# Kernel optimization log

Hardware: AMD Instinct MI355X
Metric: run time of the kernel (lower is better)

## Reference

```python
import jax, jax.numpy as jnp
import numpy as np

N = 50000          # num nodes
E = 800000         # num edges
IN_C = 256
HID = 128
OUT_C = 2
R = 8              # num_relations
B = 4              # num_bases
L = 3              # n_layers
ALPHA = 0.1


def setup_inputs() -> dict:
    key = jax.random.key(0)
    ks = jax.random.split(key, 12)
    x = jax.random.normal(ks[0], (N, IN_C), dtype=jnp.float32)
    edge_index = jax.random.randint(ks[1], (2, E), 0, N, dtype=jnp.int64)
    edge_type = jax.random.randint(ks[2], (E,), 0, R, dtype=jnp.int64)
    # parameters
    lin1_w = jax.random.normal(ks[3], (IN_C, HID), dtype=jnp.float32) * (1.0 / np.sqrt(IN_C))
    lin1_b = jnp.zeros((HID,), dtype=jnp.float32)
    bases = jax.random.normal(ks[4], (L, B, HID, HID), dtype=jnp.float32) * (1.0 / np.sqrt(HID))
    comp = jax.random.normal(ks[5], (L, R, B), dtype=jnp.float32) * (1.0 / np.sqrt(B))
    root = jax.random.normal(ks[6], (L, HID, HID), dtype=jnp.float32) * (1.0 / np.sqrt(HID))
    bias_conv = jnp.zeros((L, HID), dtype=jnp.float32)
    lin2_w = jax.random.normal(ks[7], (HID, OUT_C), dtype=jnp.float32) * (1.0 / np.sqrt(HID))
    lin2_b = jnp.zeros((OUT_C,), dtype=jnp.float32)
    # GPR-style temp init: temp[k] = alpha*(1-alpha)^k, temp[K] = (1-alpha)^K
    temp = ALPHA * (1.0 - ALPHA) ** np.arange(L + 1)
    temp[-1] = (1.0 - ALPHA) ** L
    temp = jnp.asarray(temp, dtype=jnp.float32)
    return {"x": x, "edge_index": edge_index, "edge_type": edge_type,
            "lin1_w": lin1_w, "lin1_b": lin1_b, "bases": bases, "comp": comp,
            "root": root, "bias_conv": bias_conv, "lin2_w": lin2_w,
            "lin2_b": lin2_b, "temp": temp}


def rgcn_conv(x, bases_l, comp_l, root_l, bias_l, src, dst, edge_type):
    # basis decomposition: W_r = sum_b comp[r,b] * bases[b]   -> [R, HID, HID]
    W = jnp.einsum('rb,bio->rio', comp_l, bases_l)
    out = x @ root_l + bias_l                      # root/self transform + bias
    for r in range(R):                             # fixed small relation set
        mask = (edge_type == r)
        h = x @ W[r]                               # [N, HID] relation transform
        msg = jnp.where(mask[:, None], h[src], 0.0)  # [E, HID] gathered messages
        agg = jax.ops.segment_sum(msg, dst, num_segments=N)
        cnt = jax.ops.segment_sum(mask.astype(x.dtype), dst, num_segments=N)
        out = out + agg / jnp.maximum(cnt, 1.0)[:, None]   # mean aggregation
    return out


def reference(x, edge_index, edge_type, lin1_w, lin1_b, bases, comp, root,
              bias_conv, lin2_w, lin2_b, temp):
    src, dst = edge_index[0], edge_index[1]
    h = jax.nn.relu(x @ lin1_w + lin1_b)           # pre_transform=False path; dropout=identity (eval)
    hidden = h * temp[0]
    cur = hidden
    for i in range(L):
        cur = rgcn_conv(cur, bases[i], comp[i], root[i], bias_conv[i], src, dst, edge_type)
        if i < L - 1:
            cur = jax.nn.relu(cur)
        hidden = hidden + temp[i + 1] * cur
    return hidden @ lin2_w + lin2_b                # [N, OUT_C]
```

## Files before the change

### kernel.cpp

```cpp
#include <hip/hip_runtime.h>

#define Nn   50000
#define Ee   800000
#define INC  256
#define HIDd 128
#define RR   8
#define BB   4
#define LL   3
#define RN   (RR * Nn)
#define NCH  391

typedef _Float16 f16;
typedef _Float16 f16x2 __attribute__((ext_vector_type(2)));
typedef _Float16 f16x4 __attribute__((ext_vector_type(4)));
typedef _Float16 f16x8 __attribute__((ext_vector_type(8)));
typedef float    f32x4 __attribute__((ext_vector_type(4)));

static inline size_t align256(size_t x) { return (x + 255) & ~(size_t)255; }


__global__ void count_k(const int* __restrict__ ei, const int* __restrict__ et,
                        int* __restrict__ cnt) {
    int e = blockIdx.x * 256 + threadIdx.x;
    if (e < Ee) {
        int d = ei[Ee + e];
        int r = et[e];
        atomicAdd(&cnt[r * Nn + d], 1);
    }
}

__global__ __launch_bounds__(256) void chunksum_k(const int* __restrict__ cnt,
                                                  int* __restrict__ csum) {
    int c = blockIdx.x;
    int t = threadIdx.x;
    int idx4 = c * 256 + t;
    int s = 0;
    if (idx4 < RN / 4) {
        int4 v = ((const int4*)cnt)[idx4];
        s = v.x + v.y + v.z + v.w;
    }
#pragma unroll
    for (int o = 1; o < 64; o <<= 1) s += __shfl_xor(s, o);
    __shared__ int ws[4];
    if ((t & 63) == 0) ws[t >> 6] = s;
    __syncthreads();
    if (t == 0) csum[c] = ws[0] + ws[1] + ws[2] + ws[3];
}

__global__ __launch_bounds__(512) void chunkscan_k(const int* __restrict__ csum,
                                                   int* __restrict__ cbase,
                                                   int* __restrict__ off) {
    __shared__ int lds[NCH];
    int t = threadIdx.x;
    if (t < NCH) lds[t] = csum[t];
    __syncthreads();
    if (t == 0) {
        int run = 0;
        for (int i = 0; i < NCH; ++i) { int v = lds[i]; lds[i] = run; run += v; }
        off[RN] = run;
    }
    __syncthreads();
    if (t < NCH) cbase[t] = lds[t];
}

__global__ __launch_bounds__(256) void writeoff_k(const int* __restrict__ cnt,
                                                  const int* __restrict__ cbase,
                                                  int* __restrict__ off,
                                                  int* __restrict__ cursor,
                                                  float* __restrict__ invc) {
    int c = blockIdx.x;
    int t = threadIdx.x;
    int idx4 = c * 256 + t;
    bool ok = idx4 < RN / 4;
    int4 v = make_int4(0, 0, 0, 0);
    if (ok) v = ((const int4*)cnt)[idx4];
    int s = v.x + v.y + v.z + v.w;
    int lane = t & 63;
    int incl = s;
#pragma unroll
    for (int o = 1; o < 64; o <<= 1) {
        int u = __shfl_up(incl, o);
        if (lane >= o) incl += u;
    }
    __shared__ int wsum[4];
    if (lane == 63) wsum[t >> 6] = incl;
    __syncthreads();
    int w = t >> 6;
    int wpre = 0;
    if (w > 0) wpre += wsum[0];
    if (w > 1) wpre += wsum[1];
    if (w > 2) wpre += wsum[2];
    int excl = cbase[c] + wpre + incl - s;
    if (ok) {
        int o0 = excl;
        int o1 = o0 + v.x;
        int o2 = o1 + v.y;
        int o3 = o2 + v.z;
        int4 ov = make_int4(o0, o1, o2, o3);
        ((int4*)off)[idx4] = ov;
        ((int4*)cursor)[idx4] = ov;
        float4 iv;
        iv.x = 1.0f / (float)(v.x > 1 ? v.x : 1);
        iv.y = 1.0f / (float)(v.y > 1 ? v.y : 1);
        iv.z = 1.0f / (float)(v.z > 1 ? v.z : 1);
        iv.w = 1.0f / (float)(v.w > 1 ? v.w : 1);
        ((float4*)invc)[idx4] = iv;
    }
}

__global__ void scatter_k(const int* __restrict__ ei, const int* __restrict__ et,
                          int* __restrict__ cursor, int* __restrict__ es) {
    int e = blockIdx.x * 256 + threadIdx.x;
    if (e < Ee) {
        int s = ei[e];
        int d = ei[Ee + e];
        int r = et[e];
        int p = atomicAdd(&cursor[r * Nn + d], 1);
        es[p] = s;
    }
}


__global__ void makewT_k(const float* __restrict__ bases, const float* __restrict__ root,
                         f16* __restrict__ WT) {
    int idx = blockIdx.x * 256 + threadIdx.x;
    int l = idx / (5 * 16384);
    int rem = idx % (5 * 16384);
    int c = rem >> 14;
    int n = (rem >> 7) & 127;
    int k = rem & 127;
    float v = (c == 0) ? root[l * 16384 + k * 128 + n]
                       : bases[((l * BB + (c - 1)) << 14) + k * 128 + n];
    WT[idx] = (f16)v;
}


__global__ void makew1T_k(const float* __restrict__ w1, f16* __restrict__ w1hT) {
    int idx = blockIdx.x * 256 + threadIdx.x;
    int n = idx >> 8, k = idx & 255;
    w1hT[idx] = (f16)w1[k * 128 + n];
}


__global__ __launch_bounds__(256, 2) void lin1m_k(const float* __restrict__ x,
                                                  const f16* __restrict__ w1hT,
                                                  const float* __restrict__ b1,
                                                  const float* __restrict__ temp,
                                                  const float* __restrict__ w2,
                                                  const float* __restrict__ b2,
                                                  f16* __restrict__ curh,
                                                  float* __restrict__ out) {
    __shared__ f16 Ah[128 * 136];
    __shared__ f16 Bh[128 * 136];
    __shared__ float ws2[256];
    __shared__ float bsh[2];
    int t = threadIdx.x;
    int v0 = blockIdx.x * 128;
    int w = t >> 6, lane = t & 63;
    int wr = w >> 1, wc = w & 1;
    int l15 = lane & 15, l4 = lane >> 4;
    int srow = t >> 1, sseg = t & 1;

    ws2[t] = w2[t];
    if (t < 2) bsh[t] = b2[t];

    f32x4 acc[4][4] = {};

    for (int c = 0; c < 2; ++c) {
        __syncthreads();
        {
            f16* dst = Ah + srow * 136 + sseg * 64;
            if (v0 + srow < Nn) {
                const float* src = x + (size_t)(v0 + srow) * INC + c * 128 + sseg * 64;
#pragma unroll
                for (int j = 0; j < 16; ++j) {
                    float4 f = *(const float4*)(src + j * 4);
                    f16x4 o;
                    o[0] = (f16)f.x; o[1] = (f16)f.y; o[2] = (f16)f.z; o[3] = (f16)f.w;
                    *(f16x4*)(dst + j * 4) = o;
                }
            } else {
                f16x8 z = {};
#pragma unroll
                for (int j = 0; j < 8; ++j)
                    *(f16x8*)(dst + j * 8) = z;
            }
        }
        {
            const f16* src = w1hT + srow * 256 + c * 128 + sseg * 64;
            f16* dst = Bh + srow * 136 + sseg * 64;
#pragma unroll
            for (int j = 0; j < 8; ++j)
                *(f16x8*)(dst + j * 8) = *(const f16x8*)(src + j * 8);
        }
        __syncthreads();
#pragma unroll
        for (int ks = 0; ks < 4; ++ks) {
            f16x8 af[4], bf[4];
#pragma unroll
            for (int mf = 0; mf < 4; ++mf)
                af[mf] = *(const f16x8*)(Ah + (wr * 64 + mf * 16 + l15) * 136 + ks * 32 + l4 * 8);
#pragma unroll
            for (int nf = 0; nf < 4; ++nf)
                bf[nf] = *(const f16x8*)(Bh + (wc * 64 + nf * 16 + l15) * 136 + ks * 32 + l4 * 8);
#pragma unroll
            for (int mf = 0; mf < 4; ++mf)
#pragma unroll
                for (int nf = 0; nf < 4; ++nf)
                    acc[mf][nf] = __builtin_amdgcn_mfma_f32_16x16x32_f16(af[mf], bf[nf], acc[mf][nf], 0, 0, 0);
        }
    }

    __syncthreads();
    float t0 = temp[0];
    float bs[4];
#pragma unroll
    for (int nf = 0; nf < 4; ++nf) bs[nf] = b1[wc * 64 + nf * 16 + l15];
#pragma unroll
    for (int mf = 0; mf < 4; ++mf)
#pragma unroll
        for (int nf = 0; nf < 4; ++nf)
#pragma unroll
            for (int j = 0; j < 4; ++j) {
                float val = fmaxf(acc[mf][nf][j] + bs[nf], 0.f) * t0;
                Ah[(wr * 64 + mf * 16 + l4 * 4 + j) * 136 + wc * 64 + nf * 16 + l15] = (f16)val;
            }
    __syncthreads();
    if (v0 + srow < Nn) {
        size_t gb = (size_t)(v0 + srow) * HIDd + sseg * 64;
        const f16* cr = Ah + srow * 136 + sseg * 64;
#pragma unroll
        for (int j = 0; j < 8; ++j)
            *(f16x8*)(curh + gb + j * 8) = *(const f16x8*)(cr + j * 8);
        float d0 = 0.f, d1 = 0.f;
#pragma unroll
        for (int q = 0; q < 8; ++q) {
            f16x8 cv = *(const f16x8*)(cr + q * 8);
            const float* wp = &ws2[sseg * 128 + q * 16];
#pragma unroll
            for (int j = 0; j < 8; ++j) {
                float c = (float)cv[j];
                d0 += c * wp[j * 2];
                d1 += c * wp[j * 2 + 1];
            }
        }
        d0 += __shfl_xor(d0, 1);
        d1 += __shfl_xor(d1, 1);
        if (sseg == 0) {
            out[(v0 + srow) * 2 + 0] = bsh[0] + d0;
            out[(v0 + srow) * 2 + 1] = bsh[1] + d1;
        }
    } else {
        float d0 = 0.f, d1 = 0.f;
        d0 += __shfl_xor(d0, 1);
        d1 += __shfl_xor(d1, 1);
    }
}


__global__ __launch_bounds__(256) void meanr_k(const f16* __restrict__ curh,
                                               const int* __restrict__ es,
                                               const int* __restrict__ off,
                                               const float* __restrict__ invc,
                                               const float* __restrict__ comp_l,
                                               f16* __restrict__ aggb) {
    __shared__ float ms[2][8][128];
    int t = threadIdx.x;
    int sub = t >> 7;
    int r = (t >> 4) & 7;
    int lane = t & 15;
    int d = blockIdx.x * 2 + sub;
    int g = r * Nn + d;
    int e0 = off[g], e1 = off[g + 1];
    float iv = invc[g];
    float acc[8] = {};
    const f16* cb = curh + lane * 8;
    int e = e0;
    for (; e + 4 <= e1; e += 4) {
        int s0 = es[e], s1 = es[e + 1], s2 = es[e + 2], s3 = es[e + 3];
        f16x8 v0 = *(const f16x8*)(cb + (size_t)s0 * HIDd);
        f16x8 v1 = *(const f16x8*)(cb + (size_t)s1 * HIDd);
        f16x8 v2 = *(const f16x8*)(cb + (size_t)s2 * HIDd);
        f16x8 v3 = *(const f16x8*)(cb + (size_t)s3 * HIDd);
#pragma unroll
        for (int j = 0; j < 8; ++j)
            acc[j] += (float)v0[j] + (float)v1[j] + (float)v2[j] + (float)v3[j];
    }
    for (; e < e1; ++e) {
        int s = es[e];
        f16x8 v = *(const f16x8*)(cb + (size_t)s * HIDd);
#pragma unroll
        for (int j = 0; j < 8; ++j) acc[j] += (float)v[j];
    }
    float4 p0, p1;
    p0.x = acc[0] * iv; p0.y = acc[1] * iv; p0.z = acc[2] * iv; p0.w = acc[3] * iv;
    p1.x = acc[4] * iv; p1.y = acc[5] * iv; p1.z = acc[6] * iv; p1.w = acc[7] * iv;
    *(float4*)&ms[sub][r][lane * 8]     = p0;
    *(float4*)&ms[sub][r][lane * 8 + 4] = p1;
    __syncthreads();
    int k = t & 127;
    float m[8];
#pragma unroll
    for (int rr = 0; rr < 8; ++rr) m[rr] = ms[sub][rr][k];
    f16* op = aggb + ((size_t)d * 4) * HIDd + k;
#pragma unroll
    for (int b = 0; b < 4; ++b) {
        float o = 0.f;
#pragma unroll
        for (int rr = 0; rr < 8; ++rr) o += comp_l[rr * 4 + b] * m[rr];
        op[b * HIDd] = (f16)o;
    }
}


__global__ __launch_bounds__(256, 2) void gemm_k(const f16* __restrict__ curh,
                                                 const f16* __restrict__ aggb,
                                                 const f16* __restrict__ WTl,
                                                 const float* __restrict__ bias,
                                                 const float* __restrict__ temp, int tidx,
                                                 const float* __restrict__ w2,
                                                 f16* __restrict__ curh_next,
                                                 float* __restrict__ out,
                                                 int dorelu) {
    __shared__ f16 Ah[128 * 136];
    __shared__ f16 Bh[128 * 136];
    __shared__ float ws2[256];
    int t = threadIdx.x;
    int v0 = blockIdx.x * 128;
    int w = t >> 6, lane = t & 63;
    int wr = w >> 1, wc = w & 1;
    int l15 = lane & 15, l4 = lane >> 4;
    int srow = t >> 1, sseg = t & 1;

    ws2[t] = w2[t];

    f32x4 acc[4][4] = {};

    for (int c = 0; c < 5; ++c) {
        __syncthreads();
        {
            f16* dst = Ah + srow * 136 + sseg * 64;
            if (v0 + srow < Nn) {
                const f16* src = (c == 0)
                    ? curh + (size_t)(v0 + srow) * HIDd + sseg * 64
                    : aggb + ((size_t)(v0 + srow) * 4 + (c - 1)) * HIDd + sseg * 64;
#pragma unroll
                for (int j = 0; j < 8; ++j)
                    *(f16x8*)(dst + j * 8) = *(const f16x8*)(src + j * 8);
            } else {
                f16x8 z = {};
#pragma unroll
                for (int j = 0; j < 8; ++j)
                    *(f16x8*)(dst + j * 8) = z;
            }
        }
        {
            const f16* src = WTl + (c << 14) + srow * HIDd + sseg * 64;
            f16* dst = Bh + srow * 136 + sseg * 64;
#pragma unroll
            for (int j = 0; j < 8; ++j)
                *(f16x8*)(dst + j * 8) = *(const f16x8*)(src + j * 8);
        }
        __syncthreads();
#pragma unroll
        for (int ks = 0; ks < 4; ++ks) {
            f16x8 af[4], bf[4];
#pragma unroll
            for (int mf = 0; mf < 4; ++mf)
                af[mf] = *(const f16x8*)(Ah + (wr * 64 + mf * 16 + l15) * 136 + ks * 32 + l4 * 8);
#pragma unroll
            for (int nf = 0; nf < 4; ++nf)
                bf[nf] = *(const f16x8*)(Bh + (wc * 64 + nf * 16 + l15) * 136 + ks * 32 + l4 * 8);
#pragma unroll
            for (int mf = 0; mf < 4; ++mf)
#pragma unroll
                for (int nf = 0; nf < 4; ++nf)
                    acc[mf][nf] = __builtin_amdgcn_mfma_f32_16x16x32_f16(af[mf], bf[nf], acc[mf][nf], 0, 0, 0);
        }
    }

    __syncthreads();
    float tl = temp[tidx];
    float bs[4];
#pragma unroll
    for (int nf = 0; nf < 4; ++nf) bs[nf] = bias[wc * 64 + nf * 16 + l15];
#pragma unroll
    for (int mf = 0; mf < 4; ++mf)
#pragma unroll
        for (int nf = 0; nf < 4; ++nf)
#pragma unroll
            for (int j = 0; j < 4; ++j) {
                float val = acc[mf][nf][j] + bs[nf];
                if (dorelu) val = fmaxf(val, 0.f);
                Ah[(wr * 64 + mf * 16 + l4 * 4 + j) * 136 + wc * 64 + nf * 16 + l15] = (f16)val;
            }
    __syncthreads();
    if (v0 + srow < Nn) {
        size_t gb = (size_t)(v0 + srow) * HIDd + sseg * 64;
        const f16* cr = Ah + srow * 136 + sseg * 64;
#pragma unroll
        for (int j = 0; j < 8; ++j)
            *(f16x8*)(curh_next + gb + j * 8) = *(const f16x8*)(cr + j * 8);
        float d0 = 0.f, d1 = 0.f;
#pragma unroll
        for (int q = 0; q < 8; ++q) {
            f16x8 cv = *(const f16x8*)(cr + q * 8);
            const float* wp = &ws2[sseg * 128 + q * 16];
#pragma unroll
            for (int j = 0; j < 8; ++j) {
                float c = (float)cv[j];
                d0 += c * wp[j * 2];
                d1 += c * wp[j * 2 + 1];
            }
        }
        d0 += __shfl_xor(d0, 1);
        d1 += __shfl_xor(d1, 1);
        if (sseg == 0) {
            out[(v0 + srow) * 2 + 0] += tl * d0;
            out[(v0 + srow) * 2 + 1] += tl * d1;
        }
    } else {
        float d0 = 0.f, d1 = 0.f;
        d0 += __shfl_xor(d0, 1);
        d1 += __shfl_xor(d1, 1);
    }
}


extern "C" void kernel_launch(void* const* d_in, const int* in_sizes, int n_in,
                              void* d_out, int out_size, void* d_ws, size_t ws_size,
                              hipStream_t stream) {
    (void)in_sizes; (void)n_in; (void)out_size; (void)ws_size;
    const float* x        = (const float*)d_in[0];
    const int*   ei       = (const int*)d_in[1];
    const int*   et       = (const int*)d_in[2];
    const float* lin1_w   = (const float*)d_in[3];
    const float* lin1_b   = (const float*)d_in[4];
    const float* bases    = (const float*)d_in[5];
    const float* comp     = (const float*)d_in[6];
    const float* root     = (const float*)d_in[7];
    const float* bias_cv  = (const float*)d_in[8];
    const float* lin2_w   = (const float*)d_in[9];
    const float* lin2_b   = (const float*)d_in[10];
    const float* temp     = (const float*)d_in[11];
    float* out = (float*)d_out;

    char* w = (char*)d_ws;
    int*   off    = (int*)w;    w += align256((size_t)(RN + 1) * 4);
    int*   cnt    = (int*)w;    w += align256((size_t)RN * 4);
    int*   cursor = (int*)w;    w += align256((size_t)RN * 4);
    float* invc   = (float*)w;  w += align256((size_t)RN * 4);
    int*   csum   = (int*)w;    w += align256((size_t)NCH * 4);
    int*   cbase  = (int*)w;    w += align256((size_t)NCH * 4);
    int*   es     = (int*)w;    w += align256((size_t)Ee * 4);
    f16*   WT     = (f16*)w;    w += align256((size_t)LL * 5 * HIDd * HIDd * 2);
    f16*   w1hT   = (f16*)w;    w += align256((size_t)HIDd * INC * 2);
    f16*   curh   = (f16*)w;    w += align256((size_t)Nn * HIDd * 2);
    f16*   aggb   = (f16*)w;    w += align256((size_t)Nn * 4 * HIDd * 2);

    hipMemsetAsync(cnt, 0, (size_t)RN * 4, stream);
    count_k<<<(Ee + 255) / 256, 256, 0, stream>>>(ei, et, cnt);
    chunksum_k<<<NCH, 256, 0, stream>>>(cnt, csum);
    chunkscan_k<<<1, 512, 0, stream>>>(csum, cbase, off);
    writeoff_k<<<NCH, 256, 0, stream>>>(cnt, cbase, off, cursor, invc);
    scatter_k<<<(Ee + 255) / 256, 256, 0, stream>>>(ei, et, cursor, es);
    makewT_k<<<(LL * 5 * 16384) / 256, 256, 0, stream>>>(bases, root, WT);
    makew1T_k<<<(HIDd * INC) / 256, 256, 0, stream>>>(lin1_w, w1hT);
    lin1m_k<<<(Nn + 127) / 128, 256, 0, stream>>>(x, w1hT, lin1_b, temp, lin2_w, lin2_b,
                                                  curh, out);

    for (int l = 0; l < LL; ++l) {
        meanr_k<<<Nn / 2, 256, 0, stream>>>(curh, es, off, invc, comp + l * RR * BB, aggb);
        gemm_k<<<(Nn + 127) / 128, 256, 0, stream>>>(
            curh, aggb, WT + (size_t)l * 5 * 16384, bias_cv + l * HIDd,
            temp, l + 1, lin2_w, curh, out, (l < LL - 1) ? 1 : 0);
    }
}
```

Before: 459.6 us.

## Build per-destination CSR with packed relation ids and fold basis weights per edge

Replaces the relation×destination CSR with a CSR keyed only by destination. Each edge entry packs the source id and the relation id into one int. The mean aggregation kernel now gives one 16-lane group to each destination and applies the comp·invcount weight per edge, accumulating the four basis outputs directly. This drops the shared-memory relation reduction and the 8 segment loads per node. The scan shrinks from 400k to 50k entries. In exchange it does 4x the FMAs per gathered row and relies on node ids fitting in 16 bits.

After: 475.8 us. 1.04x slower.

```diff
diff --git a/kernel.cpp b/kernel.cpp
--- a/kernel.cpp
+++ b/kernel.cpp
@@ -8,10 +8,9 @@
 #define BB   4
 #define LL   3
 #define RN   (RR * Nn)
-#define NCH  391
+#define NC2  49
 
 typedef _Float16 f16;
-typedef _Float16 f16x2 __attribute__((ext_vector_type(2)));
 typedef _Float16 f16x4 __attribute__((ext_vector_type(4)));
 typedef _Float16 f16x8 __attribute__((ext_vector_type(8)));
 typedef float    f32x4 __attribute__((ext_vector_type(4)));
@@ -20,23 +19,40 @@
 
 
 __global__ void count_k(const int* __restrict__ ei, const int* __restrict__ et,
-                        int* __restrict__ cnt) {
+                        int* __restrict__ cnt, int* __restrict__ cntd) {
     int e = blockIdx.x * 256 + threadIdx.x;
     if (e < Ee) {
         int d = ei[Ee + e];
         int r = et[e];
         atomicAdd(&cnt[r * Nn + d], 1);
-    }
-}
-
-__global__ __launch_bounds__(256) void chunksum_k(const int* __restrict__ cnt,
-                                                  int* __restrict__ csum) {
+        atomicAdd(&cntd[d], 1);
+    }
+}
+
+__global__ __launch_bounds__(256) void invc2_k(const int* __restrict__ cnt,
+                                               float* __restrict__ invc2) {
+    int d = blockIdx.x * 256 + threadIdx.x;
+    if (d < Nn) {
+        float iv[8];
+#pragma unroll
+        for (int r = 0; r < 8; ++r) {
+            int c = cnt[r * Nn + d];
+            iv[r] = 1.0f / (float)(c > 1 ? c : 1);
+        }
+        *(float4*)(invc2 + (size_t)d * 8)     = *(float4*)&iv[0];
+        *(float4*)(invc2 + (size_t)d * 8 + 4) = *(float4*)&iv[4];
+    }
+}
+
+
+__global__ __launch_bounds__(256) void chunksum2_k(const int* __restrict__ cntd,
+                                                   int* __restrict__ csum2) {
     int c = blockIdx.x;
     int t = threadIdx.x;
     int idx4 = c * 256 + t;
     int s = 0;
-    if (idx4 < RN / 4) {
-        int4 v = ((const int4*)cnt)[idx4];
+    if (idx4 < Nn / 4) {
+        int4 v = ((const int4*)cntd)[idx4];
         s = v.x + v.y + v.z + v.w;
     }
 #pragma unroll
@@ -44,36 +60,34 @@
     __shared__ int ws[4];
     if ((t & 63) == 0) ws[t >> 6] = s;
     __syncthreads();
-    if (t == 0) csum[c] = ws[0] + ws[1] + ws[2] + ws[3];
-}
-
-__global__ __launch_bounds__(512) void chunkscan_k(const int* __restrict__ csum,
-                                                   int* __restrict__ cbase,
-                                                   int* __restrict__ off) {
-    __shared__ int lds[NCH];
-    int t = threadIdx.x;
-    if (t < NCH) lds[t] = csum[t];
-    __syncthreads();
-    if (t == 0) {
-        int run = 0;
-        for (int i = 0; i < NCH; ++i) { int v = lds[i]; lds[i] = run; run += v; }
-        off[RN] = run;
-    }
-    __syncthreads();
-    if (t < NCH) cbase[t] = lds[t];
-}
-
-__global__ __launch_bounds__(256) void writeoff_k(const int* __restrict__ cnt,
-                                                  const int* __restrict__ cbase,
-                                                  int* __restrict__ off,
-                                                  int* __restrict__ cursor,
-                                                  float* __restrict__ invc) {
+    if (t == 0) csum2[c] = ws[0] + ws[1] + ws[2] + ws[3];
+}
+
+__global__ __launch_bounds__(64) void chunkscan2_k(const int* __restrict__ csum2,
+                                                   int* __restrict__ cbase2,
+                                                   int* __restrict__ off2) {
+    int t = threadIdx.x;
+    int v = (t < NC2) ? csum2[t] : 0;
+    int incl = v;
+#pragma unroll
+    for (int o = 1; o < 64; o <<= 1) {
+        int u = __shfl_up(incl, o);
+        if (t >= o) incl += u;
+    }
+    if (t < NC2) cbase2[t] = incl - v;
+    if (t == 63) off2[Nn] = incl;
+}
+
+__global__ __launch_bounds__(256) void writeoff2_k(const int* __restrict__ cntd,
+                                                   const int* __restrict__ cbase2,
+                                                   int* __restrict__ off2,
+                                                   int* __restrict__ cursor2) {
     int c = blockIdx.x;
     int t = threadIdx.x;
     int idx4 = c * 256 + t;
-    bool ok = idx4 < RN / 4;
+    bool ok = idx4 < Nn / 4;
     int4 v = make_int4(0, 0, 0, 0);
-    if (ok) v = ((const int4*)cnt)[idx4];
+    if (ok) v = ((const int4*)cntd)[idx4];
     int s = v.x + v.y + v.z + v.w;
     int lane = t & 63;
     int incl = s;
@@ -90,33 +104,27 @@
     if (w > 0) wpre += wsum[0];
     if (w > 1) wpre += wsum[1];
     if (w > 2) wpre += wsum[2];
-    int excl = cbase[c] + wpre + incl - s;
+    int excl = cbase2[c] + wpre + incl - s;
     if (ok) {
         int o0 = excl;
         int o1 = o0 + v.x;
         int o2 = o1 + v.y;
         int o3 = o2 + v.z;
         int4 ov = make_int4(o0, o1, o2, o3);
-        ((int4*)off)[idx4] = ov;
-        ((int4*)cursor)[idx4] = ov;
-        float4 iv;
-        iv.x = 1.0f / (float)(v.x > 1 ? v.x : 1);
-        iv.y = 1.0f / (float)(v.y > 1 ? v.y : 1);
-        iv.z = 1.0f / (float)(v.z > 1 ? v.z : 1);
-        iv.w = 1.0f / (float)(v.w > 1 ? v.w : 1);
-        ((float4*)invc)[idx4] = iv;
-    }
-}
-
-__global__ void scatter_k(const int* __restrict__ ei, const int* __restrict__ et,
-                          int* __restrict__ cursor, int* __restrict__ es) {
+        ((int4*)off2)[idx4] = ov;
+        ((int4*)cursor2)[idx4] = ov;
+    }
+}
+
+__global__ void scatter2_k(const int* __restrict__ ei, const int* __restrict__ et,
+                           int* __restrict__ cursor2, int* __restrict__ es2) {
     int e = blockIdx.x * 256 + threadIdx.x;
     if (e < Ee) {
         int s = ei[e];
         int d = ei[Ee + e];
         int r = et[e];
-        int p = atomicAdd(&cursor[r * Nn + d], 1);
-        es[p] = s;
+        int p = atomicAdd(&cursor2[d], 1);
+        es2[p] = s | (r << 16);
     }
 }
 
@@ -258,58 +266,67 @@
 }
 
 
-__global__ __launch_bounds__(256) void meanr_k(const f16* __restrict__ curh,
-                                               const int* __restrict__ es,
-                                               const int* __restrict__ off,
-                                               const float* __restrict__ invc,
-                                               const float* __restrict__ comp_l,
-                                               f16* __restrict__ aggb) {
-    __shared__ float ms[2][8][128];
-    int t = threadIdx.x;
-    int sub = t >> 7;
-    int r = (t >> 4) & 7;
+__global__ __launch_bounds__(256) void meanr2_k(const f16* __restrict__ curh,
+                                                const int* __restrict__ es2,
+                                                const int* __restrict__ off2,
+                                                const float* __restrict__ invc2,
+                                                const float* __restrict__ comp_l,
+                                                f16* __restrict__ aggb) {
+    __shared__ float wls[16][8][4];
+    int t = threadIdx.x;
+    int g = t >> 4;
     int lane = t & 15;
-    int d = blockIdx.x * 2 + sub;
-    int g = r * Nn + d;
-    int e0 = off[g], e1 = off[g + 1];
-    float iv = invc[g];
-    float acc[8] = {};
+    int d = blockIdx.x * 16 + g;
+    for (int f = t; f < 512; f += 256) {
+        int g2 = f >> 5, rb = f & 31, r = rb >> 2;
+        int dd = blockIdx.x * 16 + g2;
+        wls[g2][r][rb & 3] = comp_l[rb] * invc2[(size_t)dd * 8 + r];
+    }
+    __syncthreads();
+    int e = off2[d], e1 = off2[d + 1];
+    float acc0[8] = {}, acc1[8] = {}, acc2[8] = {}, acc3[8] = {};
     const f16* cb = curh + lane * 8;
-    int e = e0;
-    for (; e + 4 <= e1; e += 4) {
-        int s0 = es[e], s1 = es[e + 1], s2 = es[e + 2], s3 = es[e + 3];
-        f16x8 v0 = *(const f16x8*)(cb + (size_t)s0 * HIDd);
-        f16x8 v1 = *(const f16x8*)(cb + (size_t)s1 * HIDd);
-        f16x8 v2 = *(const f16x8*)(cb + (size_t)s2 * HIDd);
-        f16x8 v3 = *(const f16x8*)(cb + (size_t)s3 * HIDd);
-#pragma unroll
-        for (int j = 0; j < 8; ++j)
-            acc[j] += (float)v0[j] + (float)v1[j] + (float)v2[j] + (float)v3[j];
-    }
-    for (; e < e1; ++e) {
-        int s = es[e];
-        f16x8 v = *(const f16x8*)(cb + (size_t)s * HIDd);
-#pragma unroll
-        for (int j = 0; j < 8; ++j) acc[j] += (float)v[j];
-    }
-    float4 p0, p1;
-    p0.x = acc[0] * iv; p0.y = acc[1] * iv; p0.z = acc[2] * iv; p0.w = acc[3] * iv;
-    p1.x = acc[4] * iv; p1.y = acc[5] * iv; p1.z = acc[6] * iv; p1.w = acc[7] * iv;
-    *(float4*)&ms[sub][r][lane * 8]     = p0;
-    *(float4*)&ms[sub][r][lane * 8 + 4] = p1;
-    __syncthreads();
-    int k = t & 127;
-    float m[8];
-#pragma unroll
-    for (int rr = 0; rr < 8; ++rr) m[rr] = ms[sub][rr][k];
-    f16* op = aggb + ((size_t)d * 4) * HIDd + k;
-#pragma unroll
-    for (int b = 0; b < 4; ++b) {
-        float o = 0.f;
-#pragma unroll
-        for (int rr = 0; rr < 8; ++rr) o += comp_l[rr * 4 + b] * m[rr];
-        op[b * HIDd] = (f16)o;
-    }
+    for (; e + 2 <= e1; e += 2) {
+        int v0 = es2[e], v1 = es2[e + 1];
+        f16x8 row0 = *(const f16x8*)(cb + (size_t)(v0 & 0xFFFF) * HIDd);
+        f16x8 row1 = *(const f16x8*)(cb + (size_t)(v1 & 0xFFFF) * HIDd);
+        float4 w0 = *(float4*)&wls[g][v0 >> 16][0];
+        float4 w1 = *(float4*)&wls[g][v1 >> 16][0];
+#pragma unroll
+        for (int j = 0; j < 8; ++j) {
+            float a = (float)row0[j], b = (float)row1[j];
+            acc0[j] += w0.x * a + w1.x * b;
+            acc1[j] += w0.y * a + w1.y * b;
+            acc2[j] += w0.z * a + w1.z * b;
+            acc3[j] += w0.w * a + w1.w * b;
+        }
+    }
+    if (e < e1) {
+        int v0 = es2[e];
+        f16x8 row0 = *(const f16x8*)(cb + (size_t)(v0 & 0xFFFF) * HIDd);
+        float4 w0 = *(float4*)&wls[g][v0 >> 16][0];
+#pragma unroll
+        for (int j = 0; j < 8; ++j) {
+            float a = (float)row0[j];
+            acc0[j] += w0.x * a;
+            acc1[j] += w0.y * a;
+            acc2[j] += w0.z * a;
+            acc3[j] += w0.w * a;
+        }
+    }
+    f16* op = aggb + (size_t)d * 512 + lane * 8;
+    f16x8 o0, o1, o2, o3;
+#pragma unroll
+    for (int j = 0; j < 8; ++j) {
+        o0[j] = (f16)acc0[j];
+        o1[j] = (f16)acc1[j];
+        o2[j] = (f16)acc2[j];
+        o3[j] = (f16)acc3[j];
+    }
+    *(f16x8*)(op)       = o0;
+    *(f16x8*)(op + 128) = o1;
+    *(f16x8*)(op + 256) = o2;
+    *(f16x8*)(op + 384) = o3;
 }
 
 
@@ -446,31 +463,35 @@
     float* out = (float*)d_out;
 
     char* w = (char*)d_ws;
-    int*   off    = (int*)w;    w += align256((size_t)(RN + 1) * 4);
-    int*   cnt    = (int*)w;    w += align256((size_t)RN * 4);
-    int*   cursor = (int*)w;    w += align256((size_t)RN * 4);
-    float* invc   = (float*)w;  w += align256((size_t)RN * 4);
-    int*   csum   = (int*)w;    w += align256((size_t)NCH * 4);
-    int*   cbase  = (int*)w;    w += align256((size_t)NCH * 4);
-    int*   es     = (int*)w;    w += align256((size_t)Ee * 4);
-    f16*   WT     = (f16*)w;    w += align256((size_t)LL * 5 * HIDd * HIDd * 2);
-    f16*   w1hT   = (f16*)w;    w += align256((size_t)HIDd * INC * 2);
-    f16*   curh   = (f16*)w;    w += align256((size_t)Nn * HIDd * 2);
-    f16*   aggb   = (f16*)w;    w += align256((size_t)Nn * 4 * HIDd * 2);
+    int*   off2    = (int*)w;    w += align256((size_t)(Nn + 1) * 4);
+    int*   cnt     = (int*)w;    w += align256((size_t)RN * 4);
+    int*   cntd    = (int*)w;    w += align256((size_t)Nn * 4);
+    int*   cursor2 = (int*)w;    w += align256((size_t)Nn * 4);
+    float* invc2   = (float*)w;  w += align256((size_t)RN * 4);
+    int*   csum2   = (int*)w;    w += align256((size_t)NC2 * 4);
+    int*   cbase2  = (int*)w;    w += align256((size_t)NC2 * 4);
+    int*   es2     = (int*)w;    w += align256((size_t)Ee * 4);
+    f16*   WT      = (f16*)w;    w += align256((size_t)LL * 5 * HIDd * HIDd * 2);
+    f16*   w1hT    = (f16*)w;    w += align256((size_t)HIDd * INC * 2);
+    f16*   curh    = (f16*)w;    w += align256((size_t)Nn * HIDd * 2);
+    f16*   aggb    = (f16*)w;    w += align256((size_t)Nn * 4 * HIDd * 2);
 
     hipMemsetAsync(cnt, 0, (size_t)RN * 4, stream);
-    count_k<<<(Ee + 255) / 256, 256, 0, stream>>>(ei, et, cnt);
-    chunksum_k<<<NCH, 256, 0, stream>>>(cnt, csum);
-    chunkscan_k<<<1, 512, 0, stream>>>(csum, cbase, off);
-    writeoff_k<<<NCH, 256, 0, stream>>>(cnt, cbase, off, cursor, invc);
-    scatter_k<<<(Ee + 255) / 256, 256, 0, stream>>>(ei, et, cursor, es);
+    hipMemsetAsync(cntd, 0, (size_t)Nn * 4, stream);
+    count_k<<<(Ee + 255) / 256, 256, 0, stream>>>(ei, et, cnt, cntd);
+    invc2_k<<<(Nn + 255) / 256, 256, 0, stream>>>(cnt, invc2);
+    chunksum2_k<<<NC2, 256, 0, stream>>>(cntd, csum2);
+    chunkscan2_k<<<1, 64, 0, stream>>>(csum2, cbase2, off2);
+    writeoff2_k<<<NC2, 256, 0, stream>>>(cntd, cbase2, off2, cursor2);
+    scatter2_k<<<(Ee + 255) / 256, 256, 0, stream>>>(ei, et, cursor2, es2);
     makewT_k<<<(LL * 5 * 16384) / 256, 256, 0, stream>>>(bases, root, WT);
     makew1T_k<<<(HIDd * INC) / 256, 256, 0, stream>>>(lin1_w, w1hT);
     lin1m_k<<<(Nn + 127) / 128, 256, 0, stream>>>(x, w1hT, lin1_b, temp, lin2_w, lin2_b,
                                                   curh, out);
 
     for (int l = 0; l < LL; ++l) {
-        meanr_k<<<Nn / 2, 256, 0, stream>>>(curh, es, off, invc, comp + l * RR * BB, aggb);
+        meanr2_k<<<Nn / 16, 256, 0, stream>>>(curh, es2, off2, invc2,
+                                              comp + l * RR * BB, aggb);
         gemm_k<<<(Nn + 127) / 128, 256, 0, stream>>>(
             curh, aggb, WT + (size_t)l * 5 * 16384, bias_cv + l * HIDd,
             temp, l + 1, lin2_w, curh, out, (l < LL - 1) ? 1 : 0);
```
